# Optimization experiments

Hardware: AMD Instinct MI355X
Metric: run time of the kernel (lower is better)

## Reference

```python
import jax, jax.numpy as jnp
import numpy as np

NUM_HEADS = 12
CF = 2            # compression_factor
DEPTH = 3
BLOCK_DEPTH = 2
TOTAL_DEPTH_M1 = 14 - 1


def setup_inputs() -> dict:
    key = jax.random.key(0)
    k1, k2, k3, k4 = jax.random.split(key, 4)
    B, N, C = 64, 577, 768
    x = jax.random.normal(k1, (B, N, C), dtype=jnp.float32)
    qkv_w = jax.random.normal(k2, (3 * C, C), dtype=jnp.float32) * (C ** -0.5)
    proj_w = jax.random.normal(k3, (C, C), dtype=jnp.float32) * (C ** -0.5)
    proj_b = jax.random.normal(k4, (C,), dtype=jnp.float32) * 0.02
    return {"x": x, "qkv_w": qkv_w, "proj_w": proj_w, "proj_b": proj_b}


def _attn_branch(xh, qkv_w, proj_w, proj_b, zero_small):
    Bh, N, C = xh.shape
    H = NUM_HEADS
    D = C // H
    scale = D ** -0.5
    # qkv projection (no bias), split into q,k,v of shape [Bh, H, N, D]
    qkv = jnp.einsum('bnc,oc->bno', xh, qkv_w)  # [Bh, N, 3C]
    qkv = qkv.reshape(Bh, N, 3, H, D).transpose(2, 0, 3, 1, 4)  # [3, Bh, H, N, D]
    if zero_small:
        # statically zero compressed heads in q, k, v (as the torch in-place write does)
        qkv = qkv.at[:, :, H // CF:].set(0.0)
    q, k, v = qkv[0], qkv[1], qkv[2]
    attn = jnp.einsum('bhnd,bhmd->bhnm', q, k) * scale
    attn = jax.nn.softmax(attn, axis=-1)
    out = jnp.einsum('bhnm,bhmd->bhnd', attn, v)
    out = out.transpose(0, 2, 1, 3).reshape(Bh, N, C)
    out = jnp.einsum('bnc,oc->bno', out, proj_w) + proj_b
    if zero_small:
        out = out.at[:, :, C // CF:].set(0.0)
    return out


def reference(x, qkv_w, proj_w, proj_b):
    B = x.shape[0]
    x_large = _attn_branch(x[:B // 2], qkv_w, proj_w, proj_b, zero_small=False)
    if BLOCK_DEPTH <= DEPTH <= TOTAL_DEPTH_M1 - BLOCK_DEPTH:
        x_small = _attn_branch(x[B // 2:], qkv_w, proj_w, proj_b, zero_small=True)
        return jnp.concatenate((x_large, x_small), axis=0)
    return jnp.concatenate((x_large, x_large), axis=0)
```

## Files before the change

kernel.cpp:

```cpp
#include <hip/hip_runtime.h>

#define BATCH 64
#define SEQ   577
#define CDIM  768
#define NH    12
#define HD    64
#define MROWS (BATCH * SEQ)
#define KDIM  768
#define QKV_N (3 * CDIM)
#define NPAD  640
#define TQ    128
#define PS    40
#define OS    72
#define DEAD_M 18464
#define DEAD_ROW0 18560

typedef short bf16x8 __attribute__((ext_vector_type(8)));
typedef float f32x4  __attribute__((ext_vector_type(4)));

__device__ __forceinline__ unsigned short f2bf(float f) {
  unsigned int u = __float_as_uint(f);
  u += 0x7fffu + ((u >> 16) & 1u);
  return (unsigned short)(u >> 16);
}

__device__ __forceinline__ void async_ld16(const unsigned short* g, unsigned short* l) {
  __builtin_amdgcn_global_load_lds((const __attribute__((address_space(1))) void*)g,
                                   (__attribute__((address_space(3))) void*)l, 16, 0, 0);
}

__device__ __forceinline__ int xcd_swz(int id, int nwg) {
  int q = nwg >> 3, r = nwg & 7;
  int xcd = id & 7, lin = id >> 3;
  int base = (xcd < r) ? xcd * (q + 1) : r * (q + 1) + (xcd - r) * q;
  return base + lin;
}

__global__ __launch_bounds__(256) void cvt_bf16(const float* __restrict__ in,
                                                unsigned short* __restrict__ out, int n4) {
  int i = blockIdx.x * 256 + threadIdx.x;
  if (i < n4) {
    float4 f = ((const float4*)in)[i];
    ushort4 o = make_ushort4(f2bf(f.x), f2bf(f.y), f2bf(f.z), f2bf(f.w));
    ((ushort4*)out)[i] = o;
  }
}

__device__ __forceinline__ void gemm128x256_loop(
    const unsigned short* __restrict__ A,
    const unsigned short* __restrict__ Bm,
    unsigned short* sL,
    int row0, int col0,
    f32x4 (&acc)[4][4]) {
  const int tid = threadIdx.x;
  const int w = tid >> 6, lane = tid & 63;
  const int quad = lane >> 4, l16 = lane & 15;
  const int wm = w >> 2, wn = w & 3;

  const int chsw = (((lane & 7) ^ (lane >> 3)) << 3);
  int gaA0 = row0 + w * 8 + (lane >> 3);
  int gaA1 = gaA0 + 64;
  if (gaA0 >= MROWS) gaA0 = MROWS - 1;
  if (gaA1 >= MROWS) gaA1 = MROWS - 1;
  const unsigned short* aS0 = A + (size_t)gaA0 * KDIM + chsw;
  const unsigned short* aS1 = A + (size_t)gaA1 * KDIM + chsw;
  const int gb = col0 + w * 8 + (lane >> 3);
  const unsigned short* bS = Bm + (size_t)gb * KDIM + chsw;
  const int dstA = tid * 8;
  const int dstB = 8192 + tid * 8;

  const int swzA = ((quad ^ (l16 & 7)) << 3);
  const int arow = (wm * 64 + l16) * 64;
  const int brow = 8192 + (wn * 64 + l16) * 64;

  #pragma unroll 2
  for (int t = 0; t < 12; ++t) {
    __syncthreads();
    {
      const unsigned short* a0 = aS0 + t * 64;
      const unsigned short* a1 = aS1 + t * 64;
      const unsigned short* b0 = bS + t * 64;
      async_ld16(a0, sL + dstA);
      async_ld16(a1, sL + dstA + 4096);
      async_ld16(b0,                  sL + dstB);
      async_ld16(b0 + 64 * KDIM,      sL + dstB + 4096);
      async_ld16(b0 + 128 * KDIM,     sL + dstB + 8192);
      async_ld16(b0 + 192 * KDIM,     sL + dstB + 12288);
    }
    asm volatile("s_waitcnt vmcnt(0)" ::: "memory");
    __syncthreads();
    #pragma unroll
    for (int ks = 0; ks < 2; ++ks) {
      const int sz = swzA ^ (ks << 5);
      bf16x8 af[4], bfv[4];
      #pragma unroll
      for (int i = 0; i < 4; ++i) af[i] = *(const bf16x8*)&sL[arow + i * 1024 + sz];
      #pragma unroll
      for (int j = 0; j < 4; ++j) bfv[j] = *(const bf16x8*)&sL[brow + j * 1024 + sz];
      #pragma unroll
      for (int i = 0; i < 4; ++i)
        #pragma unroll
        for (int j = 0; j < 4; ++j)
          acc[i][j] = __builtin_amdgcn_mfma_f32_16x16x32_bf16(af[i], bfv[j], acc[i][j], 0, 0, 0);
    }
  }
}

__global__ __launch_bounds__(512, 4) void gemm_qkv(
    const unsigned short* __restrict__ A,
    const unsigned short* __restrict__ Bm,
    unsigned short* __restrict__ qb,
    unsigned short* __restrict__ kb,
    unsigned short* __restrict__ vb) {
  const int wg = xcd_swz(blockIdx.x, 289 * 9);
  const int mt = wg / 9, nt = wg - mt * 9;
  const int row0 = mt * 128, col0 = nt * 256;
  if (row0 >= DEAD_ROW0 && (col0 % CDIM) == 512) return;

  __shared__ unsigned short sL[32768];
  f32x4 acc[4][4] = {};
  gemm128x256_loop(A, Bm, sL, row0, col0, acc);

  __syncthreads();

  const int tid = threadIdx.x;
  const int w = tid >> 6, lane = tid & 63;
  const int quad = lane >> 4, l16 = lane & 15;
  const int wm = w >> 2, wn = w & 3;

  const int wcol = col0 + wn * 64;
  const int three = wcol / CDIM;
  const int rem = wcol - three * CDIM;
  const int h = rem >> 6;
  unsigned short* dst = (three == 0) ? qb : (three == 1) ? kb : vb;
  const float sc = (three == 0) ? 0.180336878f : 1.0f;
  if ((row0 + wm * 64) >= DEAD_M && h >= 6) return;

  unsigned short* so = sL + w * 4096;
  #pragma unroll
  for (int i = 0; i < 4; ++i)
    #pragma unroll
    for (int j = 0; j < 4; ++j)
      #pragma unroll
      for (int r = 0; r < 4; ++r) {
        int rr = i * 16 + quad * 4 + r;
        so[rr * 64 + (((j * 2 + (l16 >> 3)) ^ (rr & 7)) << 3) + (l16 & 7)] =
            f2bf(acc[i][j][r] * sc);
      }
  #pragma unroll
  for (int it = 0; it < 8; ++it) {
    int c = it * 64 + lane;
    int rr = c >> 3, s8 = c & 7;
    int m = row0 + wm * 64 + rr;
    if (m < MROWS) {
      int b = m / SEQ, n = m - b * SEQ;
      *(int4*)&dst[((((size_t)b * NH + h) * SEQ + n) << 6) + s8 * 8] =
          *(const int4*)&so[rr * 64 + ((s8 ^ (rr & 7)) << 3)];
    }
  }
}

__global__ __launch_bounds__(512) void transpose_v(
    const unsigned short* __restrict__ v,
    unsigned short* __restrict__ vt) {
  const int bh = blockIdx.y;
  const int b = bh / NH, h = bh - b * NH;
  if (b >= 32 && h >= 6) return;
  const int t = blockIdx.x;
  const int tid = threadIdx.x;
  const int w = tid >> 6, lane = tid & 63;
  int n = t * 64 + lane;
  bf16x8 vv = {};
  if (n < SEQ)
    vv = *(const bf16x8*)&v[(size_t)bh * (SEQ * HD) + n * HD + w * 8];
  unsigned short* dst = vt + (size_t)bh * (HD * NPAD) + (w * 8) * NPAD + t * 64 + lane;
  #pragma unroll
  for (int j = 0; j < 8; j++)
    dst[j * NPAD] = ((const unsigned short*)&vv)[j];
}

__global__ __launch_bounds__(256, 4) void flash_attn(
    const unsigned short* __restrict__ q,
    const unsigned short* __restrict__ k,
    const unsigned short* __restrict__ vt,
    unsigned short* __restrict__ attn) {
  const int id = blockIdx.x;
  const int bh8 = id / 40;
  const int rem = id - bh8 * 40;
  const int qt = rem >> 3;
  const int bh = bh8 * 8 + (rem & 7);
  const int b = bh / NH, h = bh - b * NH;
  const int tid = threadIdx.x;
  const int w = tid >> 6, lane = tid & 63;
  const int quad = lane >> 4, l16 = lane & 15;

  if (b >= 32 && h >= 6) {
    for (int it = tid; it < TQ * 8; it += 256) {
      int r = it >> 3, c8 = (it & 7) * 8;
      int n = qt * TQ + r;
      if (n < SEQ)
        *(int4*)&attn[(b * SEQ + n) * CDIM + h * 64 + c8] = make_int4(0, 0, 0, 0);
    }
    return;
  }

  __shared__ unsigned short sK[2 * 64 * 32];
  __shared__ unsigned short sVt[2 * 64 * 32];
  __shared__ unsigned short sP[4][64 * PS];

  const unsigned short* qbase = q + (size_t)bh * (SEQ * HD);
  const unsigned short* kbase = k + (size_t)bh * (SEQ * HD);
  const unsigned short* vtbase = vt + (size_t)bh * (HD * NPAD);

  const int fsw = ((quad ^ ((l16 >> 1) & 3)) << 3);

  bf16x8 aq[2][2];
  #pragma unroll
  for (int g = 0; g < 2; g++) {
    int qr = qt * TQ + w * 32 + g * 16 + l16;
    if (qr > SEQ - 1) qr = SEQ - 1;
    aq[g][0] = *(const bf16x8*)&qbase[qr * HD + quad * 8];
    aq[g][1] = *(const bf16x8*)&qbase[qr * HD + 32 + quad * 8];
  }

  f32x4 oacc[2][4] = {};
  f32x4 lacc[2] = {};

  const short ONE = (short)0x3F80;

  for (int t = 0; t < 10; t++) {
    __syncthreads();
    #pragma unroll
    for (int c = 0; c < 2; c++) {
      int rI = tid >> 2;
      int c4s = (tid & 3) ^ ((tid >> 3) & 3);
      int base = c * 2048 + (tid & ~63) * 8;
      int kr = t * 64 + rI; if (kr > SEQ - 1) kr = SEQ - 1;
      async_ld16(kbase + kr * HD + c * 32 + c4s * 8, sK + base);
      async_ld16(vtbase + rI * NPAD + t * 64 + c * 32 + c4s * 8, sVt + base);
    }
    __syncthreads();

    bf16x8 bk[4][2];
    #pragma unroll
    for (int nt = 0; nt < 4; nt++) {
      bk[nt][0] = *(const bf16x8*)&sK[0 * 2048 + (nt * 16 + l16) * 32 + fsw];
      bk[nt][1] = *(const bf16x8*)&sK[1 * 2048 + (nt * 16 + l16) * 32 + fsw];
    }

    bf16x8 ones0, ones1;
    if (t < 9) {
      #pragma unroll
      for (int j = 0; j < 8; j++) { ones0[j] = ONE; ones1[j] = ONE; }
    } else {
      bf16x8 z = {};
      ones0 = z; ones1 = z;
      ones0[0] = (quad == 0) ? ONE : (short)0;
    }

    #pragma unroll
    for (int g = 0; g < 2; g++) {
      f32x4 s[4];
      #pragma unroll
      for (int nt = 0; nt < 4; nt++) {
        f32x4 z = {};
        z = __builtin_amdgcn_mfma_f32_16x16x32_bf16(aq[g][0], bk[nt][0], z, 0, 0, 0);
        z = __builtin_amdgcn_mfma_f32_16x16x32_bf16(aq[g][1], bk[nt][1], z, 0, 0, 0);
        s[nt] = z;
      }
      #pragma unroll
      for (int nt = 0; nt < 4; nt++)
        #pragma unroll
        for (int r = 0; r < 4; r++)
          sP[w][((g * 2 + (nt >> 1)) * 16 + quad * 4 + r) * PS + (nt & 1) * 16 + l16] =
              f2bf(__builtin_exp2f(s[nt][r]));
    }

    #pragma unroll
    for (int g = 0; g < 2; g++) {
      bf16x8 pa0 = *(const bf16x8*)&sP[w][((g * 2 + 0) * 16 + l16) * PS + quad * 8];
      bf16x8 pa1 = *(const bf16x8*)&sP[w][((g * 2 + 1) * 16 + l16) * PS + quad * 8];
      #pragma unroll
      for (int dt = 0; dt < 4; dt++) {
        bf16x8 bv0 = *(const bf16x8*)&sVt[0 * 2048 + (dt * 16 + l16) * 32 + fsw];
        bf16x8 bv1 = *(const bf16x8*)&sVt[1 * 2048 + (dt * 16 + l16) * 32 + fsw];
        oacc[g][dt] = __builtin_amdgcn_mfma_f32_16x16x32_bf16(pa0, bv0, oacc[g][dt], 0, 0, 0);
        oacc[g][dt] = __builtin_amdgcn_mfma_f32_16x16x32_bf16(pa1, bv1, oacc[g][dt], 0, 0, 0);
      }
      lacc[g] = __builtin_amdgcn_mfma_f32_16x16x32_bf16(pa0, ones0, lacc[g], 0, 0, 0);
      lacc[g] = __builtin_amdgcn_mfma_f32_16x16x32_bf16(pa1, ones1, lacc[g], 0, 0, 0);
    }
  }

  unsigned short* so = &sP[w][0];
  #pragma unroll
  for (int g = 0; g < 2; g++)
    #pragma unroll
    for (int r = 0; r < 4; r++) {
      float inv = 1.0f / lacc[g][r];
      #pragma unroll
      for (int dt = 0; dt < 4; dt++)
        so[(g * 16 + quad * 4 + r) * OS + dt * 16 + l16] = f2bf(oacc[g][dt][r] * inv);
    }
  #pragma unroll
  for (int it = 0; it < 4; it++) {
    int chunk = it * 64 + lane;
    int row = chunk >> 3, c8 = chunk & 7;
    int n = qt * TQ + w * 32 + row;
    if (n < SEQ)
      *(int4*)&attn[(b * SEQ + n) * CDIM + h * 64 + c8 * 8] =
          *(const int4*)&so[row * OS + c8 * 8];
  }
}

__global__ __launch_bounds__(512, 4) void gemm_proj(
    const unsigned short* __restrict__ A,
    const unsigned short* __restrict__ Bm,
    const float* __restrict__ bias,
    float* __restrict__ out) {
  const int wg = xcd_swz(blockIdx.x, 289 * 3);
  const int mt = wg / 3, nt = wg - mt * 3;
  const int row0 = mt * 128, col0 = nt * 256;
  const int tid = threadIdx.x;

  if (row0 >= DEAD_ROW0 && col0 >= (CDIM / 2)) {
    float4 z4 = make_float4(0.f, 0.f, 0.f, 0.f);
    #pragma unroll
    for (int it = 0; it < 16; ++it) {
      int idx = it * 512 + tid;
      int r = idx >> 6, c4 = idx & 63;
      int m = row0 + r;
      if (m < MROWS)
        *(float4*)&out[(size_t)m * CDIM + col0 + c4 * 4] = z4;
    }
    return;
  }

  __shared__ unsigned short sL[24576];
  f32x4 acc[4][4] = {};
  gemm128x256_loop(A, Bm, sL, row0, col0, acc);

  const int w = tid >> 6, lane = tid & 63;
  const int quad = lane >> 4, l16 = lane & 15;
  const int wm = w >> 2, wn = w & 3;

  float bv[4];
  #pragma unroll
  for (int nf = 0; nf < 4; ++nf) bv[nf] = bias[col0 + wn * 64 + nf * 16 + l16];

  #pragma unroll
  for (int mf = 0; mf < 4; ++mf) {
    int mb = row0 + wm * 64 + mf * 16 + quad * 4;
    #pragma unroll
    for (int nf = 0; nf < 4; ++nf) {
      int col = col0 + wn * 64 + nf * 16 + l16;
      bool maskc = (col >= (CDIM / 2));
      #pragma unroll
      for (int r = 0; r < 4; ++r) {
        int m = mb + r;
        if (m < MROWS) {
          float val = acc[mf][nf][r] + bv[nf];
          if (m >= DEAD_M && maskc) val = 0.f;
          out[(size_t)m * CDIM + col] = val;
        }
      }
    }
  }
}

extern "C" void kernel_launch(void* const* d_in, const int* in_sizes, int n_in,
                              void* d_out, int out_size, void* d_ws, size_t ws_size,
                              hipStream_t stream) {
  const float* x      = (const float*)d_in[0];
  const float* qkv_w  = (const float*)d_in[1];
  const float* proj_w = (const float*)d_in[2];
  const float* proj_b = (const float*)d_in[3];
  float* out = (float*)d_out;

  size_t off = 0;
  auto alloc = [&](size_t bytes) {
    void* p = (char*)d_ws + off;
    off += (bytes + 255) & ~(size_t)255;
    return p;
  };
  const size_t XE = (size_t)MROWS * KDIM;
  unsigned short* xb   = (unsigned short*)alloc(XE * 2);
  unsigned short* wqb  = (unsigned short*)alloc((size_t)QKV_N * KDIM * 2);
  unsigned short* wpb  = (unsigned short*)alloc((size_t)CDIM * KDIM * 2);
  unsigned short* qb   = (unsigned short*)alloc(XE * 2);
  unsigned short* kb   = (unsigned short*)alloc(XE * 2);
  unsigned short* vb   = (unsigned short*)alloc(XE * 2);
  unsigned short* vtb  = (unsigned short*)alloc((size_t)BATCH * NH * HD * NPAD * 2);
  unsigned short* attnb = xb;
  (void)ws_size;

  cvt_bf16<<<(int)(XE / 4 / 256), 256, 0, stream>>>(x, xb, (int)(XE / 4));
  cvt_bf16<<<(QKV_N * KDIM / 4) / 256, 256, 0, stream>>>(qkv_w, wqb, QKV_N * KDIM / 4);
  cvt_bf16<<<(CDIM * KDIM / 4) / 256, 256, 0, stream>>>(proj_w, wpb, CDIM * KDIM / 4);

  gemm_qkv<<<dim3(289 * 9), 512, 0, stream>>>(xb, wqb, qb, kb, vb);

  transpose_v<<<dim3(10, BATCH * NH), 512, 0, stream>>>(vb, vtb);

  flash_attn<<<(BATCH * NH / 8) * 40, 256, 0, stream>>>(qb, kb, vtb, attnb);

  gemm_proj<<<dim3(289 * 3), 512, 0, stream>>>(attnb, wpb, proj_b, out);
}
```

Before: 520.8 us.

## Use 32x32x16 MFMA in GEMMs and double-buffer K/V tiles in attention

The shared GEMM loop switches from 16x16x32 to 32x32x16 bf16 MFMA tiles, which halves the number of LDS fragment loads per MFMA flop. The QKV and projection epilogues are remapped to the 32x32 accumulator layout. The attention kernel double-buffers the K and V^T LDS tiles so the next tile's async load overlaps compute on the current one, and it reorders the PV MFMAs to reuse the V fragments. The cost is twice the LDS for K and V, which may lower occupancy, plus new index math in the epilogues that could be wrong.

```diff
diff --git a/kernel.cpp b/kernel.cpp
--- a/kernel.cpp
+++ b/kernel.cpp
@@ -17,6 +17,7 @@
 
 typedef short bf16x8 __attribute__((ext_vector_type(8)));
 typedef float f32x4  __attribute__((ext_vector_type(4)));
+typedef float f32x16 __attribute__((ext_vector_type(16)));
 
 __device__ __forceinline__ unsigned short f2bf(float f) {
   unsigned int u = __float_as_uint(f);
@@ -51,10 +52,10 @@
     const unsigned short* __restrict__ Bm,
     unsigned short* sL,
     int row0, int col0,
-    f32x4 (&acc)[4][4]) {
+    f32x16 (&acc)[2][2]) {
   const int tid = threadIdx.x;
   const int w = tid >> 6, lane = tid & 63;
-  const int quad = lane >> 4, l16 = lane & 15;
+  const int l31 = lane & 31, hh = lane >> 5;
   const int wm = w >> 2, wn = w & 3;
 
   const int chsw = (((lane & 7) ^ (lane >> 3)) << 3);
@@ -69,9 +70,9 @@
   const int dstA = tid * 8;
   const int dstB = 8192 + tid * 8;
 
-  const int swzA = ((quad ^ (l16 & 7)) << 3);
-  const int arow = (wm * 64 + l16) * 64;
-  const int brow = 8192 + (wn * 64 + l16) * 64;
+  const int arow = (wm * 64 + l31) * 64;
+  const int brow = 8192 + (wn * 64 + l31) * 64;
+  const int l7 = l31 & 7;
 
   #pragma unroll 2
   for (int t = 0; t < 12; ++t) {
@@ -90,18 +91,16 @@
     asm volatile("s_waitcnt vmcnt(0)" ::: "memory");
     __syncthreads();
     #pragma unroll
-    for (int ks = 0; ks < 2; ++ks) {
-      const int sz = swzA ^ (ks << 5);
-      bf16x8 af[4], bfv[4];
-      #pragma unroll
-      for (int i = 0; i < 4; ++i) af[i] = *(const bf16x8*)&sL[arow + i * 1024 + sz];
-      #pragma unroll
-      for (int j = 0; j < 4; ++j) bfv[j] = *(const bf16x8*)&sL[brow + j * 1024 + sz];
-      #pragma unroll
-      for (int i = 0; i < 4; ++i)
-        #pragma unroll
-        for (int j = 0; j < 4; ++j)
-          acc[i][j] = __builtin_amdgcn_mfma_f32_16x16x32_bf16(af[i], bfv[j], acc[i][j], 0, 0, 0);
+    for (int ks = 0; ks < 4; ++ks) {
+      const int co = ((((ks << 1) | hh) ^ l7) << 3);
+      bf16x8 a0 = *(const bf16x8*)&sL[arow + co];
+      bf16x8 a1 = *(const bf16x8*)&sL[arow + 2048 + co];
+      bf16x8 b0 = *(const bf16x8*)&sL[brow + co];
+      bf16x8 b1 = *(const bf16x8*)&sL[brow + 2048 + co];
+      acc[0][0] = __builtin_amdgcn_mfma_f32_32x32x16_bf16(a0, b0, acc[0][0], 0, 0, 0);
+      acc[0][1] = __builtin_amdgcn_mfma_f32_32x32x16_bf16(a0, b1, acc[0][1], 0, 0, 0);
+      acc[1][0] = __builtin_amdgcn_mfma_f32_32x32x16_bf16(a1, b0, acc[1][0], 0, 0, 0);
+      acc[1][1] = __builtin_amdgcn_mfma_f32_32x32x16_bf16(a1, b1, acc[1][1], 0, 0, 0);
     }
   }
 }
@@ -118,14 +117,14 @@
   if (row0 >= DEAD_ROW0 && (col0 % CDIM) == 512) return;
 
   __shared__ unsigned short sL[32768];
-  f32x4 acc[4][4] = {};
+  f32x16 acc[2][2] = {};
   gemm128x256_loop(A, Bm, sL, row0, col0, acc);
 
   __syncthreads();
 
   const int tid = threadIdx.x;
   const int w = tid >> 6, lane = tid & 63;
-  const int quad = lane >> 4, l16 = lane & 15;
+  const int l31 = lane & 31, hh = lane >> 5;
   const int wm = w >> 2, wn = w & 3;
 
   const int wcol = col0 + wn * 64;
@@ -138,14 +137,14 @@
 
   unsigned short* so = sL + w * 4096;
   #pragma unroll
-  for (int i = 0; i < 4; ++i)
-    #pragma unroll
-    for (int j = 0; j < 4; ++j)
-      #pragma unroll
-      for (int r = 0; r < 4; ++r) {
-        int rr = i * 16 + quad * 4 + r;
-        so[rr * 64 + (((j * 2 + (l16 >> 3)) ^ (rr & 7)) << 3) + (l16 & 7)] =
-            f2bf(acc[i][j][r] * sc);
+  for (int i = 0; i < 2; ++i)
+    #pragma unroll
+    for (int j = 0; j < 2; ++j)
+      #pragma unroll
+      for (int r = 0; r < 16; ++r) {
+        int rr = i * 32 + (r & 3) + 8 * (r >> 2) + 4 * hh;
+        int slot = (j * 4 + (l31 >> 3)) ^ (rr & 7);
+        so[rr * 64 + (slot << 3) + (l31 & 7)] = f2bf(acc[i][j][r] * sc);
       }
   #pragma unroll
   for (int it = 0; it < 8; ++it) {
@@ -204,8 +203,8 @@
     return;
   }
 
-  __shared__ unsigned short sK[2 * 64 * 32];
-  __shared__ unsigned short sVt[2 * 64 * 32];
+  __shared__ unsigned short sK[2][2 * 64 * 32];
+  __shared__ unsigned short sVt[2][2 * 64 * 32];
   __shared__ unsigned short sP[4][64 * PS];
 
   const unsigned short* qbase = q + (size_t)bh * (SEQ * HD);
@@ -213,6 +212,18 @@
   const unsigned short* vtbase = vt + (size_t)bh * (HD * NPAD);
 
   const int fsw = ((quad ^ ((l16 >> 1) & 3)) << 3);
+
+  auto fstage = [&](int t, int s) {
+    #pragma unroll
+    for (int c = 0; c < 2; c++) {
+      int rI = tid >> 2;
+      int c4s = (tid & 3) ^ ((tid >> 3) & 3);
+      int base = c * 2048 + (tid & ~63) * 8;
+      int kr = t * 64 + rI; if (kr > SEQ - 1) kr = SEQ - 1;
+      async_ld16(kbase + kr * HD + c * 32 + c4s * 8, &sK[s][base]);
+      async_ld16(vtbase + rI * NPAD + t * 64 + c * 32 + c4s * 8, &sVt[s][base]);
+    }
+  };
 
   bf16x8 aq[2][2];
   #pragma unroll
@@ -228,24 +239,18 @@
 
   const short ONE = (short)0x3F80;
 
+  fstage(0, 0);
   for (int t = 0; t < 10; t++) {
+    const int s = t & 1;
+    asm volatile("s_waitcnt vmcnt(0)" ::: "memory");
     __syncthreads();
-    #pragma unroll
-    for (int c = 0; c < 2; c++) {
-      int rI = tid >> 2;
-      int c4s = (tid & 3) ^ ((tid >> 3) & 3);
-      int base = c * 2048 + (tid & ~63) * 8;
-      int kr = t * 64 + rI; if (kr > SEQ - 1) kr = SEQ - 1;
-      async_ld16(kbase + kr * HD + c * 32 + c4s * 8, sK + base);
-      async_ld16(vtbase + rI * NPAD + t * 64 + c * 32 + c4s * 8, sVt + base);
-    }
-    __syncthreads();
+    if (t < 9) fstage(t + 1, s ^ 1);
 
     bf16x8 bk[4][2];
     #pragma unroll
     for (int nt = 0; nt < 4; nt++) {
-      bk[nt][0] = *(const bf16x8*)&sK[0 * 2048 + (nt * 16 + l16) * 32 + fsw];
-      bk[nt][1] = *(const bf16x8*)&sK[1 * 2048 + (nt * 16 + l16) * 32 + fsw];
+      bk[nt][0] = *(const bf16x8*)&sK[s][0 * 2048 + (nt * 16 + l16) * 32 + fsw];
+      bk[nt][1] = *(const bf16x8*)&sK[s][1 * 2048 + (nt * 16 + l16) * 32 + fsw];
     }
 
     bf16x8 ones0, ones1;
@@ -260,35 +265,42 @@
 
     #pragma unroll
     for (int g = 0; g < 2; g++) {
-      f32x4 s[4];
+      f32x4 sacc[4];
       #pragma unroll
       for (int nt = 0; nt < 4; nt++) {
         f32x4 z = {};
         z = __builtin_amdgcn_mfma_f32_16x16x32_bf16(aq[g][0], bk[nt][0], z, 0, 0, 0);
         z = __builtin_amdgcn_mfma_f32_16x16x32_bf16(aq[g][1], bk[nt][1], z, 0, 0, 0);
-        s[nt] = z;
+        sacc[nt] = z;
       }
       #pragma unroll
       for (int nt = 0; nt < 4; nt++)
         #pragma unroll
         for (int r = 0; r < 4; r++)
           sP[w][((g * 2 + (nt >> 1)) * 16 + quad * 4 + r) * PS + (nt & 1) * 16 + l16] =
-              f2bf(__builtin_exp2f(s[nt][r]));
-    }
-
+              f2bf(__builtin_exp2f(sacc[nt][r]));
+    }
+
+    bf16x8 pa[2][2];
     #pragma unroll
     for (int g = 0; g < 2; g++) {
-      bf16x8 pa0 = *(const bf16x8*)&sP[w][((g * 2 + 0) * 16 + l16) * PS + quad * 8];
-      bf16x8 pa1 = *(const bf16x8*)&sP[w][((g * 2 + 1) * 16 + l16) * PS + quad * 8];
-      #pragma unroll
-      for (int dt = 0; dt < 4; dt++) {
-        bf16x8 bv0 = *(const bf16x8*)&sVt[0 * 2048 + (dt * 16 + l16) * 32 + fsw];
-        bf16x8 bv1 = *(const bf16x8*)&sVt[1 * 2048 + (dt * 16 + l16) * 32 + fsw];
-        oacc[g][dt] = __builtin_amdgcn_mfma_f32_16x16x32_bf16(pa0, bv0, oacc[g][dt], 0, 0, 0);
-        oacc[g][dt] = __builtin_amdgcn_mfma_f32_16x16x32_bf16(pa1, bv1, oacc[g][dt], 0, 0, 0);
+      pa[g][0] = *(const bf16x8*)&sP[w][((g * 2 + 0) * 16 + l16) * PS + quad * 8];
+      pa[g][1] = *(const bf16x8*)&sP[w][((g * 2 + 1) * 16 + l16) * PS + quad * 8];
+    }
+    #pragma unroll
+    for (int dt = 0; dt < 4; dt++) {
+      bf16x8 bv0 = *(const bf16x8*)&sVt[s][0 * 2048 + (dt * 16 + l16) * 32 + fsw];
+      bf16x8 bv1 = *(const bf16x8*)&sVt[s][1 * 2048 + (dt * 16 + l16) * 32 + fsw];
+      #pragma unroll
+      for (int g = 0; g < 2; g++) {
+        oacc[g][dt] = __builtin_amdgcn_mfma_f32_16x16x32_bf16(pa[g][0], bv0, oacc[g][dt], 0, 0, 0);
+        oacc[g][dt] = __builtin_amdgcn_mfma_f32_16x16x32_bf16(pa[g][1], bv1, oacc[g][dt], 0, 0, 0);
       }
-      lacc[g] = __builtin_amdgcn_mfma_f32_16x16x32_bf16(pa0, ones0, lacc[g], 0, 0, 0);
-      lacc[g] = __builtin_amdgcn_mfma_f32_16x16x32_bf16(pa1, ones1, lacc[g], 0, 0, 0);
+    }
+    #pragma unroll
+    for (int g = 0; g < 2; g++) {
+      lacc[g] = __builtin_amdgcn_mfma_f32_16x16x32_bf16(pa[g][0], ones0, lacc[g], 0, 0, 0);
+      lacc[g] = __builtin_amdgcn_mfma_f32_16x16x32_bf16(pa[g][1], ones1, lacc[g], 0, 0, 0);
     }
   }
 
@@ -337,35 +349,33 @@
   }
 
   __shared__ unsigned short sL[24576];
-  f32x4 acc[4][4] = {};
+  f32x16 acc[2][2] = {};
   gemm128x256_loop(A, Bm, sL, row0, col0, acc);
 
   const int w = tid >> 6, lane = tid & 63;
-  const int quad = lane >> 4, l16 = lane & 15;
+  const int l31 = lane & 31, hh = lane >> 5;
   const int wm = w >> 2, wn = w & 3;
 
-  float bv[4];
-  #pragma unroll
-  for (int nf = 0; nf < 4; ++nf) bv[nf] = bias[col0 + wn * 64 + nf * 16 + l16];
-
-  #pragma unroll
-  for (int mf = 0; mf < 4; ++mf) {
-    int mb = row0 + wm * 64 + mf * 16 + quad * 4;
-    #pragma unroll
-    for (int nf = 0; nf < 4; ++nf) {
-      int col = col0 + wn * 64 + nf * 16 + l16;
+  float bv[2];
+  #pragma unroll
+  for (int j = 0; j < 2; ++j) bv[j] = bias[col0 + wn * 64 + j * 32 + l31];
+
+  #pragma unroll
+  for (int i = 0; i < 2; ++i)
+    #pragma unroll
+    for (int j = 0; j < 2; ++j) {
+      int col = col0 + wn * 64 + j * 32 + l31;
       bool maskc = (col >= (CDIM / 2));
       #pragma unroll
-      for (int r = 0; r < 4; ++r) {
-        int m = mb + r;
+      for (int r = 0; r < 16; ++r) {
+        int m = row0 + wm * 64 + i * 32 + (r & 3) + 8 * (r >> 2) + 4 * hh;
         if (m < MROWS) {
-          float val = acc[mf][nf][r] + bv[nf];
+          float val = acc[i][j][r] + bv[j];
           if (m >= DEAD_M && maskc) val = 0.f;
           out[(size_t)m * CDIM + col] = val;
         }
       }
     }
-  }
 }
 
 extern "C" void kernel_launch(void* const* d_in, const int* in_sizes, int n_in,
```

Result: slower. 543.9 us (+4.4%).

## Load K and V tiles directly from global into registers, drop LDS staging

Applied to the files above, without the earlier changes.

The attention kernel no longer stages K and V^T tiles through shared memory with async loads and two block barriers per iteration. Each wave now reads its K and V fragments straight from global memory (relying on L1/L2 for reuse across the four waves), and the score and PV MFMA loops are regrouped so more independent MFMAs are issued together. This removes block-wide synchronisation and LDS traffic, but each wave now fetches the same K/V data separately, which increases global/cache traffic and exposes load latency.

```diff
diff --git a/kernel.cpp b/kernel.cpp
--- a/kernel.cpp
+++ b/kernel.cpp
@@ -204,15 +204,11 @@
     return;
   }
 
-  __shared__ unsigned short sK[2 * 64 * 32];
-  __shared__ unsigned short sVt[2 * 64 * 32];
   __shared__ unsigned short sP[4][64 * PS];
 
   const unsigned short* qbase = q + (size_t)bh * (SEQ * HD);
   const unsigned short* kbase = k + (size_t)bh * (SEQ * HD);
   const unsigned short* vtbase = vt + (size_t)bh * (HD * NPAD);
-
-  const int fsw = ((quad ^ ((l16 >> 1) & 3)) << 3);
 
   bf16x8 aq[2][2];
   #pragma unroll
@@ -229,23 +225,12 @@
   const short ONE = (short)0x3F80;
 
   for (int t = 0; t < 10; t++) {
-    __syncthreads();
-    #pragma unroll
-    for (int c = 0; c < 2; c++) {
-      int rI = tid >> 2;
-      int c4s = (tid & 3) ^ ((tid >> 3) & 3);
-      int base = c * 2048 + (tid & ~63) * 8;
-      int kr = t * 64 + rI; if (kr > SEQ - 1) kr = SEQ - 1;
-      async_ld16(kbase + kr * HD + c * 32 + c4s * 8, sK + base);
-      async_ld16(vtbase + rI * NPAD + t * 64 + c * 32 + c4s * 8, sVt + base);
-    }
-    __syncthreads();
-
     bf16x8 bk[4][2];
     #pragma unroll
     for (int nt = 0; nt < 4; nt++) {
-      bk[nt][0] = *(const bf16x8*)&sK[0 * 2048 + (nt * 16 + l16) * 32 + fsw];
-      bk[nt][1] = *(const bf16x8*)&sK[1 * 2048 + (nt * 16 + l16) * 32 + fsw];
+      int kr = t * 64 + nt * 16 + l16; if (kr > SEQ - 1) kr = SEQ - 1;
+      bk[nt][0] = *(const bf16x8*)&kbase[kr * HD + quad * 8];
+      bk[nt][1] = *(const bf16x8*)&kbase[kr * HD + 32 + quad * 8];
     }
 
     bf16x8 ones0, ones1;
@@ -258,37 +243,50 @@
       ones0[0] = (quad == 0) ? ONE : (short)0;
     }
 
-    #pragma unroll
-    for (int g = 0; g < 2; g++) {
-      f32x4 s[4];
+    f32x4 sc2[2][4];
+    #pragma unroll
+    for (int g = 0; g < 2; g++)
       #pragma unroll
       for (int nt = 0; nt < 4; nt++) {
         f32x4 z = {};
         z = __builtin_amdgcn_mfma_f32_16x16x32_bf16(aq[g][0], bk[nt][0], z, 0, 0, 0);
         z = __builtin_amdgcn_mfma_f32_16x16x32_bf16(aq[g][1], bk[nt][1], z, 0, 0, 0);
-        s[nt] = z;
+        sc2[g][nt] = z;
       }
+
+    #pragma unroll
+    for (int g = 0; g < 2; g++)
       #pragma unroll
       for (int nt = 0; nt < 4; nt++)
         #pragma unroll
         for (int r = 0; r < 4; r++)
           sP[w][((g * 2 + (nt >> 1)) * 16 + quad * 4 + r) * PS + (nt & 1) * 16 + l16] =
-              f2bf(__builtin_exp2f(s[nt][r]));
-    }
-
+              f2bf(__builtin_exp2f(sc2[g][nt][r]));
+
+    bf16x8 bv[4][2];
+    #pragma unroll
+    for (int dt = 0; dt < 4; dt++) {
+      bv[dt][0] = *(const bf16x8*)&vtbase[(dt * 16 + l16) * NPAD + t * 64 + quad * 8];
+      bv[dt][1] = *(const bf16x8*)&vtbase[(dt * 16 + l16) * NPAD + t * 64 + 32 + quad * 8];
+    }
+
+    bf16x8 pa[2][2];
     #pragma unroll
     for (int g = 0; g < 2; g++) {
-      bf16x8 pa0 = *(const bf16x8*)&sP[w][((g * 2 + 0) * 16 + l16) * PS + quad * 8];
-      bf16x8 pa1 = *(const bf16x8*)&sP[w][((g * 2 + 1) * 16 + l16) * PS + quad * 8];
-      #pragma unroll
-      for (int dt = 0; dt < 4; dt++) {
-        bf16x8 bv0 = *(const bf16x8*)&sVt[0 * 2048 + (dt * 16 + l16) * 32 + fsw];
-        bf16x8 bv1 = *(const bf16x8*)&sVt[1 * 2048 + (dt * 16 + l16) * 32 + fsw];
-        oacc[g][dt] = __builtin_amdgcn_mfma_f32_16x16x32_bf16(pa0, bv0, oacc[g][dt], 0, 0, 0);
-        oacc[g][dt] = __builtin_amdgcn_mfma_f32_16x16x32_bf16(pa1, bv1, oacc[g][dt], 0, 0, 0);
+      pa[g][0] = *(const bf16x8*)&sP[w][((g * 2 + 0) * 16 + l16) * PS + quad * 8];
+      pa[g][1] = *(const bf16x8*)&sP[w][((g * 2 + 1) * 16 + l16) * PS + quad * 8];
+    }
+    #pragma unroll
+    for (int dt = 0; dt < 4; dt++)
+      #pragma unroll
+      for (int g = 0; g < 2; g++) {
+        oacc[g][dt] = __builtin_amdgcn_mfma_f32_16x16x32_bf16(pa[g][0], bv[dt][0], oacc[g][dt], 0, 0, 0);
+        oacc[g][dt] = __builtin_amdgcn_mfma_f32_16x16x32_bf16(pa[g][1], bv[dt][1], oacc[g][dt], 0, 0, 0);
       }
-      lacc[g] = __builtin_amdgcn_mfma_f32_16x16x32_bf16(pa0, ones0, lacc[g], 0, 0, 0);
-      lacc[g] = __builtin_amdgcn_mfma_f32_16x16x32_bf16(pa1, ones1, lacc[g], 0, 0, 0);
+    #pragma unroll
+    for (int g = 0; g < 2; g++) {
+      lacc[g] = __builtin_amdgcn_mfma_f32_16x16x32_bf16(pa[g][0], ones0, lacc[g], 0, 0, 0);
+      lacc[g] = __builtin_amdgcn_mfma_f32_16x16x32_bf16(pa[g][1], ones1, lacc[g], 0, 0, 0);
     }
   }
 
```

After: 665.5 us. 1.28x slower.
